# Kernel optimization log

Hardware: AMD Instinct MI355X
Metric: run time of the kernel (lower is better)

The kernel has to match this reference:

```python
import jax, jax.numpy as jnp
import numpy as np
from jax import lax

B, S = 64, 3000
Q_SIZES = [(4, 16), (16, 32), (32, 64), (64, 128), (128, 256)]
NUM_CLASS = 10


def setup_inputs() -> dict:
    key = jax.random.key(0)
    ks = iter(jax.random.split(key, 40))

    def g(shape, scale=0.05):
        return jax.random.normal(next(ks), shape, dtype=jnp.float32) * scale

    d = {}
    d["x"] = jax.random.normal(next(ks), (B, S, 1), dtype=jnp.float32)
    # vanilla tanh RNN, hidden=4
    d["wih"] = g((4, 1))
    d["whh"] = g((4, 4))
    d["bih"] = g((4,))
    d["bhh"] = g((4,))
    # 5 QRNN layers: affine to (Z, F) of width 2*out
    for i, (ni, no) in enumerate(Q_SIZES, 1):
        d[f"qw{i}"] = g((ni, 2 * no))
        d[f"qb{i}"] = g((2 * no,))
    # trailing MLP (weights stored as (in, out))
    d["w1"] = g((3000, 1024))
    d["b1"] = g((1024,))
    d["w2"] = g((1024, 128))
    d["b2"] = g((128,))
    d["w3"] = g((128, NUM_CLASS))
    d["b3"] = g((NUM_CLASS,))
    return d


def _rnn_tanh(x, wih, whh, bih, bhh):
    # x: (B, S, 1) -> (B, S, 4)
    pre = jnp.einsum('bsi,hi->bsh', x, wih) + bih + bhh  # input part precomputed
    b = x.shape[0]

    def step(h, p):
        h = jnp.tanh(p + h @ whh.T)
        return h, h

    _, hs = lax.scan(step, jnp.zeros((b, whh.shape[0]), x.dtype), jnp.moveaxis(pre, 1, 0))
    return jnp.moveaxis(hs, 0, 1)


def _qrnn(x, w, bq):
    # x: (B, S, Cin); fo-pool: h_t = f_t*h_{t-1} + (1-f_t)*z_t
    H = w.shape[1] // 2
    zf = x @ w + bq  # (B, S, 2H) -- one big GEMM, recurrence is elementwise
    z = jnp.tanh(zf[..., :H])
    f = jax.nn.sigmoid(zf[..., H:])
    b = x.shape[0]

    def step(h, zft):
        z_t, f_t = zft
        h = f_t * h + (1.0 - f_t) * z_t
        return h, h

    _, hs = lax.scan(step, jnp.zeros((b, H), x.dtype),
                     (jnp.moveaxis(z, 1, 0), jnp.moveaxis(f, 1, 0)))
    return jnp.moveaxis(hs, 0, 1)  # (B, S, H)


def reference(x, wih, whh, bih, bhh,
              qw1, qb1, qw2, qb2, qw3, qb3, qw4, qb4, qw5, qb5,
              w1, b1, w2, b2, w3, b3):
    h = _rnn_tanh(x, wih, whh, bih, bhh)          # (B, S, 4)
    for w, bq in ((qw1, qb1), (qw2, qb2), (qw3, qb3), (qw4, qb4), (qw5, qb5)):
        h = _qrnn(h, w, bq)                        # (B, S, C)
    # AdaptiveAvgPool1d(1) on (B, S, C): mean over channel axis -> (B, S)
    h = h.mean(axis=-1)                            # (B, 3000)
    h = jax.nn.relu(h @ w1 + b1)                   # dropout = identity (eval)
    h = jax.nn.relu(h @ w2 + b2)
    h = jax.nn.relu(h @ w3 + b3)
    return h
```

## Files before the change

### kernel.cpp

```cpp
#include <hip/hip_runtime.h>

#define DEVI __device__ __forceinline__

static constexpr int Bb = 64;
static constexpr int Ss = 3000;
static constexpr int Mm = Bb * Ss;
static constexpr int NCH = 12;
static constexpr int CLEN = 250;
static constexpr int WARM = 64;
static constexpr int NCK = 12;
static constexpr int RCH = 60;
static constexpr int RCLEN = 50;
static constexpr int RWARM = 32;

typedef short bs8 __attribute__((ext_vector_type(8)));
typedef float f32x4 __attribute__((ext_vector_type(4)));

DEVI float fast_tanh(float x) {
    float e = __expf(2.0f * x);
    return 1.0f - 2.0f * __builtin_amdgcn_rcpf(e + 1.0f);
}
DEVI float fast_sigmoid(float x) {
    return __builtin_amdgcn_rcpf(1.0f + __expf(-x));
}
DEVI unsigned short f2bf(float f) {
    unsigned u = __float_as_uint(f);
    u += 0x7FFF + ((u >> 16) & 1);
    return (unsigned short)(u >> 16);
}
DEVI float bf2f(unsigned short h) { return __uint_as_float(((unsigned)h) << 16); }

__global__ __launch_bounds__(64) void rnn_kernel2(const float* __restrict__ x,
                                                  const float* __restrict__ wih,
                                                  const float* __restrict__ whh,
                                                  const float* __restrict__ bih,
                                                  const float* __restrict__ bhh,
                                                  float* __restrict__ hout) {
    __shared__ float xs[Ss];
    int b = blockIdx.x;
    for (int i = threadIdx.x; i < Ss / 4; i += 64) {
        *(float4*)&xs[i * 4] = *(const float4*)&x[b * Ss + i * 4];
    }
    __syncthreads();
    int ck = threadIdx.x;
    if (ck >= RCH) return;
    float w[4][4], wi[4], bc[4];
#pragma unroll
    for (int j = 0; j < 4; ++j) {
        wi[j] = wih[j];
        bc[j] = bih[j] + bhh[j];
#pragma unroll
        for (int i = 0; i < 4; ++i) w[j][i] = whh[j * 4 + i];
    }
    float h0 = 0.f, h1 = 0.f, h2 = 0.f, h3 = 0.f;
    int sc = ck * RCLEN;
    int sb = ck ? (sc - RWARM) : 0;
#pragma unroll 4
    for (int s = sb; s < sc; ++s) {
        float xv = xs[s];
        float n0 = fast_tanh(fmaf(xv, wi[0], bc[0]) + w[0][0]*h0 + w[0][1]*h1 + w[0][2]*h2 + w[0][3]*h3);
        float n1 = fast_tanh(fmaf(xv, wi[1], bc[1]) + w[1][0]*h0 + w[1][1]*h1 + w[1][2]*h2 + w[1][3]*h3);
        float n2 = fast_tanh(fmaf(xv, wi[2], bc[2]) + w[2][0]*h0 + w[2][1]*h1 + w[2][2]*h2 + w[2][3]*h3);
        float n3 = fast_tanh(fmaf(xv, wi[3], bc[3]) + w[3][0]*h0 + w[3][1]*h1 + w[3][2]*h2 + w[3][3]*h3);
        h0 = n0; h1 = n1; h2 = n2; h3 = n3;
    }
#pragma unroll 5
    for (int s = sc; s < sc + RCLEN; ++s) {
        float xv = xs[s];
        float n0 = fast_tanh(fmaf(xv, wi[0], bc[0]) + w[0][0]*h0 + w[0][1]*h1 + w[0][2]*h2 + w[0][3]*h3);
        float n1 = fast_tanh(fmaf(xv, wi[1], bc[1]) + w[1][0]*h0 + w[1][1]*h1 + w[1][2]*h2 + w[1][3]*h3);
        float n2 = fast_tanh(fmaf(xv, wi[2], bc[2]) + w[2][0]*h0 + w[2][1]*h1 + w[2][2]*h2 + w[2][3]*h3);
        float n3 = fast_tanh(fmaf(xv, wi[3], bc[3]) + w[3][0]*h0 + w[3][1]*h1 + w[3][2]*h2 + w[3][3]*h3);
        h0 = n0; h1 = n1; h2 = n2; h3 = n3;
        *(float4*)&hout[(size_t)(b * Ss + s) * 4] = make_float4(h0, h1, h2, h3);
    }
}

__global__ void prep_wfrag(const float* __restrict__ W, short* __restrict__ Wh,
                           short* __restrict__ Wl, int K, int N2) {
    int total = K * N2;
    int NS = K / 32;
    for (int t = blockIdx.x * blockDim.x + threadIdx.x; t < total; t += gridDim.x * blockDim.x) {
        int n = t / K, k = t % K;
        float w = W[(size_t)k * N2 + n];
        int frag = n >> 4;
        int s = k >> 5;
        int lane = (n & 15) | (((k >> 3) & 3) << 4);
        int elem = k & 7;
        size_t off = (((size_t)(frag * NS + s)) * 64 + lane) * 8 + elem;
        unsigned short h = f2bf(w);
        Wh[off] = (short)h;
        Wl[off] = (short)f2bf(w - bf2f(h));
    }
}

template <int K, int H, bool POOL>
__global__ __launch_bounds__(512) void qrnn_fused(const short* __restrict__ Ap,
                                                  const short* __restrict__ Wh,
                                                  const short* __restrict__ Wl,
                                                  const float* __restrict__ bias,
                                                  short* __restrict__ Hout,
                                                  float* __restrict__ pooled) {
    constexpr int SUBR = 32;
    constexpr int NS = K / 32;
    constexpr int WN = (H / 16 < 8) ? (H / 16) : 8;
    constexpr int WR = 8 / WN;
    constexpr int NZF = H / (16 * WN);
    constexpr int RPW = SUBR / WR;
    constexpr int RF = RPW / 16;
    constexpr int LDA = K + 8;
    constexpr int ZP = H + 4;

    __shared__ short As[SUBR * LDA];
    __shared__ unsigned zfs[SUBR][ZP];

    const int tid = threadIdx.x;
    const int lane = tid & 63;
    const int w = tid >> 6;
    const int rg = w / WN, cg = w % WN;
    const int l15 = lane & 15, lh = lane >> 4;

    const int bi = blockIdx.x;
    const int b = bi / NCK, ck = bi % NCK;
    const int s0 = ck * 256;

    float hscan = 0.f;

    const int tstart = (ck == 0) ? 0 : -2;
    for (int t = tstart; t < 8; ++t) {
        const int st = s0 + t * SUBR;
        if (st >= Ss) break;
        const size_t grow0 = (size_t)b * Ss + st;

        {
            constexpr int CH = K / 8;
            for (int q = tid; q < SUBR * CH; q += 512) {
                int r = q / CH, hq = q % CH;
                *(bs8*)&As[r * LDA + hq * 8] = *(const bs8*)&Ap[(grow0 + r) * K + hq * 8];
            }
        }
        __syncthreads();

        f32x4 acc[RF][2 * NZF];
#pragma unroll
        for (int i = 0; i < RF; ++i)
#pragma unroll
            for (int j = 0; j < 2 * NZF; ++j) acc[i][j] = (f32x4)0.f;

#pragma unroll
        for (int s = 0; s < NS; ++s) {
            bs8 ah[RF];
#pragma unroll
            for (int i = 0; i < RF; ++i)
                ah[i] = *(const bs8*)&As[(rg * RPW + i * 16 + l15) * LDA + s * 32 + lh * 8];
#pragma unroll
            for (int nz = 0; nz < NZF; ++nz) {
                int fz = cg * NZF + nz;
                int ff = H / 16 + fz;
                bs8 bzh = *(const bs8*)&Wh[(((size_t)fz * NS + s) * 64 + lane) * 8];
                bs8 bzl = *(const bs8*)&Wl[(((size_t)fz * NS + s) * 64 + lane) * 8];
                bs8 bfh = *(const bs8*)&Wh[(((size_t)ff * NS + s) * 64 + lane) * 8];
                bs8 bfl = *(const bs8*)&Wl[(((size_t)ff * NS + s) * 64 + lane) * 8];
#pragma unroll
                for (int i = 0; i < RF; ++i) {
                    acc[i][nz] = __builtin_amdgcn_mfma_f32_16x16x32_bf16(ah[i], bzh, acc[i][nz], 0, 0, 0);
                    acc[i][nz] = __builtin_amdgcn_mfma_f32_16x16x32_bf16(ah[i], bzl, acc[i][nz], 0, 0, 0);
                    acc[i][NZF + nz] = __builtin_amdgcn_mfma_f32_16x16x32_bf16(ah[i], bfh, acc[i][NZF + nz], 0, 0, 0);
                    acc[i][NZF + nz] = __builtin_amdgcn_mfma_f32_16x16x32_bf16(ah[i], bfl, acc[i][NZF + nz], 0, 0, 0);
                }
            }
        }

#pragma unroll
        for (int nz = 0; nz < NZF; ++nz) {
            int c = cg * (16 * NZF) + nz * 16 + l15;
            float bz = bias[c], bfv = bias[H + c];
#pragma unroll
            for (int i = 0; i < RF; ++i) {
                int rbase = rg * RPW + i * 16 + lh * 4;
#pragma unroll
                for (int r = 0; r < 4; ++r) {
                    float zv = fast_tanh(acc[i][nz][r] + bz);
                    float fv = fast_sigmoid(acc[i][NZF + nz][r] + bfv);
                    zfs[rbase + r][c] = (((unsigned)f2bf(zv)) << 16) | (unsigned)f2bf(fv);
                }
            }
        }
        __syncthreads();

        if (tid < H) {
            int c = tid;
            float h = hscan;
#pragma unroll 8
            for (int r = 0; r < SUBR; ++r) {
                unsigned u = zfs[r][c];
                float z = bf2f((unsigned short)(u >> 16));
                float f = bf2f((unsigned short)(u & 0xFFFF));
                h = fmaf(f, h - z, z);
                if (POOL) {
                    zfs[r][c] = __float_as_uint(h);
                } else {
                    int s = st + r;
                    if (t >= 0 && s < Ss)
                        Hout[((size_t)b * Ss + s) * H + c] = (short)f2bf(h);
                }
            }
            hscan = h;
        }
        __syncthreads();

        if (POOL) {
            if (t >= 0) {
#pragma unroll
                for (int rr = 0; rr < SUBR / 8; ++rr) {
                    int r = w * (SUBR / 8) + rr;
                    float sum = __uint_as_float(zfs[r][lane]) +
                                __uint_as_float(zfs[r][lane + 64]) +
                                __uint_as_float(zfs[r][lane + 128]) +
                                __uint_as_float(zfs[r][lane + 192]);
#pragma unroll
                    for (int off = 32; off >= 1; off >>= 1)
                        sum += __shfl_xor(sum, off, 64);
                    int s = st + r;
                    if (lane == 0 && s < Ss)
                        pooled[(size_t)b * Ss + s] = sum * (1.f / 256.f);
                }
            }
            __syncthreads();
        }
    }
}

template <int K>
__global__ __launch_bounds__(256) void qrnn_gemm(const float* __restrict__ A,
                                                 const float* __restrict__ W,
                                                 const float* __restrict__ bias,
                                                 float* __restrict__ ZF,
                                                 int Nfull, int Wout, int Hg, int z0, int f0) {
    constexpr int BM = 64, BN = 64;
    constexpr int BK = (K < 32) ? K : 32;
    __shared__ float As[BK][BM + 4];
    __shared__ float Bs[BK][BN];
    const int tid = threadIdx.x;
    const int tx = tid % 16, ty = tid / 16;
    const int m0 = blockIdx.x * BM;
    const int n0 = blockIdx.y * BN;
    float acc[4][4] = {};

    for (int k0 = 0; k0 < K; k0 += BK) {
        constexpr int KQ = BK / 4;
        constexpr int AV = BM * KQ;
        for (int v = tid; v < AV; v += 256) {
            int m = v / KQ, kq = v % KQ;
            float4 av = *(const float4*)&A[(size_t)(m0 + m) * K + k0 + kq * 4];
            As[kq * 4 + 0][m] = av.x;
            As[kq * 4 + 1][m] = av.y;
            As[kq * 4 + 2][m] = av.z;
            As[kq * 4 + 3][m] = av.w;
        }
        constexpr int BV = BK * 16;
        for (int v = tid; v < BV; v += 256) {
            int ki = v / 16, nq = v % 16;
            int j = n0 + nq * 4;
            float4 bv = make_float4(0.f, 0.f, 0.f, 0.f);
            if (j < Wout) {
                int wc = (j < Hg) ? (z0 + j) : (f0 + (j - Hg));
                bv = *(const float4*)&W[(size_t)(k0 + ki) * Nfull + wc];
            }
            *(float4*)&Bs[ki][nq * 4] = bv;
        }
        __syncthreads();
#pragma unroll
        for (int kk = 0; kk < BK; ++kk) {
            float a[4];
#pragma unroll
            for (int i = 0; i < 4; ++i) a[i] = As[kk][ty * 4 + i];
            float4 bv = *(const float4*)&Bs[kk][tx * 4];
            float bb[4] = {bv.x, bv.y, bv.z, bv.w};
#pragma unroll
            for (int i = 0; i < 4; ++i)
#pragma unroll
                for (int j = 0; j < 4; ++j) acc[i][j] = fmaf(a[i], bb[j], acc[i][j]);
        }
        __syncthreads();
    }
    int jb = n0 + tx * 4;
    if (jb < Wout) {
        bool isz = jb < Hg;
#pragma unroll
        for (int i = 0; i < 4; ++i) {
            int gm = m0 + ty * 4 + i;
            float o[4];
#pragma unroll
            for (int jj = 0; jj < 4; ++jj) {
                int j = jb + jj;
                int wc = isz ? (z0 + j) : (f0 + (j - Hg));
                float v = acc[i][jj] + bias[wc];
                o[jj] = isz ? fast_tanh(v) : fast_sigmoid(v);
            }
            *(float4*)&ZF[(size_t)gm * Wout + jb] = make_float4(o[0], o[1], o[2], o[3]);
        }
    }
}

__global__ void scan_f2c(const float* __restrict__ zf, float* __restrict__ hout,
                         int Hg, int W2, int Hfull, int ch0) {
    int id = blockIdx.x * blockDim.x + threadIdx.x;
    int total = Bb * NCH * Hg;
    if (id >= total) return;
    int c = id % Hg;
    int p = id / Hg;
    int b = p / NCH, ck = p % NCH;
    int sc = ck * CLEN;
    float h = 0.f;
    if (ck) {
#pragma unroll 4
        for (int s = sc - WARM; s < sc; ++s) {
            size_t base = (size_t)(b * Ss + s) * W2;
            float z = zf[base + c], f = zf[base + Hg + c];
            h = fmaf(f, h - z, z);
        }
    }
#pragma unroll 5
    for (int s = sc; s < sc + CLEN; ++s) {
        size_t base = (size_t)(b * Ss + s) * W2;
        float z = zf[base + c], f = zf[base + Hg + c];
        h = fmaf(f, h - z, z);
        hout[(size_t)(b * Ss + s) * Hfull + ch0 + c] = h;
    }
}

__global__ void scan_f2p(const float* __restrict__ zf, short* __restrict__ Ahp,
                         int Hg, int W2, int Kn, int ch0) {
    int id = blockIdx.x * blockDim.x + threadIdx.x;
    int total = Bb * NCH * Hg;
    if (id >= total) return;
    int c = id % Hg;
    int p = id / Hg;
    int b = p / NCH, ck = p % NCH;
    int sc = ck * CLEN;
    float h = 0.f;
    if (ck) {
#pragma unroll 4
        for (int s = sc - WARM; s < sc; ++s) {
            size_t base = (size_t)(b * Ss + s) * W2;
            float z = zf[base + c], f = zf[base + Hg + c];
            h = fmaf(f, h - z, z);
        }
    }
#pragma unroll 5
    for (int s = sc; s < sc + CLEN; ++s) {
        size_t base = (size_t)(b * Ss + s) * W2;
        float z = zf[base + c], f = zf[base + Hg + c];
        h = fmaf(f, h - z, z);
        Ahp[(size_t)(b * Ss + s) * Kn + ch0 + c] = (short)f2bf(h);
    }
}

__global__ __launch_bounds__(256) void mlp1_kernel(const float* __restrict__ xp,
                                                   const float* __restrict__ w1,
                                                   float* __restrict__ parts) {
    const int n0 = blockIdx.x * 64;
    const int ks = blockIdx.y;
    const int kbeg = ks * 250;
    const int nl = threadIdx.x % 64, mg = threadIdx.x / 64;
    __shared__ float xs[50][68];
    float acc[16] = {};
    for (int kc = 0; kc < 5; ++kc) {
        int k0 = kbeg + kc * 50;
        __syncthreads();
        for (int idx = threadIdx.x; idx < 64 * 50; idx += 256) {
            int r = idx / 50, cc = idx % 50;
            xs[cc][r] = xp[r * Ss + k0 + cc];
        }
        __syncthreads();
#pragma unroll 5
        for (int kk = 0; kk < 50; ++kk) {
            float wv = w1[(size_t)(k0 + kk) * 1024 + n0 + nl];
#pragma unroll
            for (int q = 0; q < 4; ++q) {
                float4 xv = *(const float4*)&xs[kk][mg * 16 + q * 4];
                acc[q * 4 + 0] = fmaf(xv.x, wv, acc[q * 4 + 0]);
                acc[q * 4 + 1] = fmaf(xv.y, wv, acc[q * 4 + 1]);
                acc[q * 4 + 2] = fmaf(xv.z, wv, acc[q * 4 + 2]);
                acc[q * 4 + 3] = fmaf(xv.w, wv, acc[q * 4 + 3]);
            }
        }
    }
#pragma unroll
    for (int i = 0; i < 16; ++i) {
        int m = mg * 16 + i;
        parts[((size_t)ks * 64 + m) * 1024 + n0 + nl] = acc[i];
    }
}

__global__ void mlp1_reduce(const float* __restrict__ parts, const float* __restrict__ b1,
                            float* __restrict__ h1) {
    int id = blockIdx.x * 256 + threadIdx.x;
    int n = id % 1024, m = id / 1024;
    float s = b1[n];
#pragma unroll
    for (int ks = 0; ks < 12; ++ks) s += parts[((size_t)ks * 64 + m) * 1024 + n];
    h1[id] = fmaxf(s, 0.f);
}

__global__ void mlp2_kernel(const float* __restrict__ h1, const float* __restrict__ w2,
                            const float* __restrict__ b2, float* __restrict__ h2) {
    int m = blockIdx.x, n = threadIdx.x;
    float acc = 0.f;
#pragma unroll 8
    for (int k = 0; k < 1024; ++k) acc = fmaf(h1[m * 1024 + k], w2[k * 128 + n], acc);
    h2[m * 128 + n] = fmaxf(acc + b2[n], 0.f);
}

__global__ void mlp3_kernel(const float* __restrict__ h2, const float* __restrict__ w3,
                            const float* __restrict__ b3, float* __restrict__ out) {
    int t = threadIdx.x;
    if (t >= 640) return;
    int m = t / 10, n = t % 10;
    float acc = 0.f;
#pragma unroll
    for (int k = 0; k < 128; ++k) acc = fmaf(h2[m * 128 + k], w3[k * 10 + n], acc);
    out[t] = fmaxf(acc + b3[n], 0.f);
}

extern "C" void kernel_launch(void* const* d_in, const int* in_sizes, int n_in,
                              void* d_out, int out_size, void* d_ws, size_t ws_size,
                              hipStream_t stream) {
    const float* x   = (const float*)d_in[0];
    const float* wih = (const float*)d_in[1];
    const float* whh = (const float*)d_in[2];
    const float* bih = (const float*)d_in[3];
    const float* bhh = (const float*)d_in[4];
    const float* qw[5] = {(const float*)d_in[5], (const float*)d_in[7], (const float*)d_in[9],
                          (const float*)d_in[11], (const float*)d_in[13]};
    const float* qb[5] = {(const float*)d_in[6], (const float*)d_in[8], (const float*)d_in[10],
                          (const float*)d_in[12], (const float*)d_in[14]};
    const float* w1 = (const float*)d_in[15];
    const float* b1 = (const float*)d_in[16];
    const float* w2 = (const float*)d_in[17];
    const float* b2 = (const float*)d_in[18];
    const float* w3 = (const float*)d_in[19];
    const float* b3 = (const float*)d_in[20];
    float* out = (float*)d_out;

    char* ws = (char*)d_ws;
    size_t off = 0;
    auto carve = [&](size_t sz) {
        char* q = ws + off;
        off += (sz + 255) & ~size_t(255);
        return q;
    };
    float* h4    = (float*)carve((size_t)Mm * 4 * 4);
    float* h16   = (float*)carve((size_t)Mm * 16 * 4);
    float* zf32  = (float*)carve((size_t)Mm * 64 * 4);
    short* p32   = (short*)carve((size_t)(Mm + 128) * 32 * 2);
    short* p64   = (short*)carve((size_t)(Mm + 128) * 64 * 2);
    short* p128  = (short*)carve((size_t)(Mm + 128) * 128 * 2);
    float* pooled = (float*)carve((size_t)Bb * Ss * 4);
    float* parts  = (float*)carve(12ull * 64 * 1024 * 4);
    float* h1m    = (float*)carve(64ull * 1024 * 4);
    float* h2m    = (float*)carve(64ull * 128 * 4);
    short* wh2 = (short*)carve(4096 * 2);
    short* wl2 = (short*)carve(4096 * 2);
    short* wh3 = (short*)carve(16384 * 2);
    short* wl3 = (short*)carve(16384 * 2);
    short* wh4 = (short*)carve(65536 * 2);
    short* wl4 = (short*)carve(65536 * 2);
    (void)ws_size;

    prep_wfrag<<<8,  256, 0, stream>>>(qw[2], wh2, wl2, 32, 128);
    prep_wfrag<<<16, 256, 0, stream>>>(qw[3], wh3, wl3, 64, 256);
    prep_wfrag<<<64, 256, 0, stream>>>(qw[4], wh4, wl4, 128, 512);

    rnn_kernel2<<<Bb, 64, 0, stream>>>(x, wih, whh, bih, bhh, h4);

    {
        dim3 grid(Mm / 64, 1);
        qrnn_gemm<4><<<grid, 256, 0, stream>>>(h4, qw[0], qb[0], zf32, 32, 32, 16, 0, 16);
        int total = Bb * NCH * 16;
        scan_f2c<<<(total + 255) / 256, 256, 0, stream>>>(zf32, h16, 16, 32, 16, 0);
    }
    {
        dim3 grid(Mm / 64, 1);
        qrnn_gemm<16><<<grid, 256, 0, stream>>>(h16, qw[1], qb[1], zf32, 64, 64, 32, 0, 32);
        int total = Bb * NCH * 32;
        scan_f2p<<<(total + 255) / 256, 256, 0, stream>>>(zf32, p32, 32, 64, 32, 0);
    }
    qrnn_fused<32, 64, false><<<Bb * NCK, 512, 0, stream>>>(p32, wh2, wl2, qb[2], p64, nullptr);
    qrnn_fused<64, 128, false><<<Bb * NCK, 512, 0, stream>>>(p64, wh3, wl3, qb[3], p128, nullptr);
    qrnn_fused<128, 256, true><<<Bb * NCK, 512, 0, stream>>>(p128, wh4, wl4, qb[4], nullptr, pooled);

    mlp1_kernel<<<dim3(16, 12), 256, 0, stream>>>(pooled, w1, parts);
    mlp1_reduce<<<256, 256, 0, stream>>>(parts, b1, h1m);
    mlp2_kernel<<<64, 128, 0, stream>>>(h1m, w2, b2, h2m);
    mlp3_kernel<<<1, 640, 0, stream>>>(h2m, w3, b3, out);
    (void)in_sizes; (void)n_in; (void)out_size;
}
```

Before: 598.4 us.

## Double-buffer activation tiles, preload weights to registers, widen QRNN subtiles

The fused QRNN kernel now loads its hi/lo bf16 weight fragments into registers once per block instead of re-reading them from global memory on every subtile. Activation tiles are double-buffered in shared memory so the next tile's load is issued while the current tile's MFMAs run. The subtile height grows from 32 to 64 rows, and the warm-up history shrinks from two 32-row subtiles to one 64-row subtile. The aim is less global weight traffic and fewer barrier stalls, at the cost of much higher register pressure for large K/H layers and twice the LDS for the A tile.

```diff
diff --git a/kernel.cpp b/kernel.cpp
--- a/kernel.cpp
+++ b/kernel.cpp
@@ -101,7 +101,8 @@
                                                   const float* __restrict__ bias,
                                                   short* __restrict__ Hout,
                                                   float* __restrict__ pooled) {
-    constexpr int SUBR = 32;
+    constexpr int SUBR = 64;
+    constexpr int NT = 256 / SUBR;
     constexpr int NS = K / 32;
     constexpr int WN = (H / 16 < 8) ? (H / 16) : 8;
     constexpr int WR = 8 / WN;
@@ -110,8 +111,9 @@
     constexpr int RF = RPW / 16;
     constexpr int LDA = K + 8;
     constexpr int ZP = H + 4;
-
-    __shared__ short As[SUBR * LDA];
+    constexpr int CH = K / 8;
+
+    __shared__ short As[2 * SUBR * LDA];
     __shared__ unsigned zfs[SUBR][ZP];
 
     const int tid = threadIdx.x;
@@ -124,60 +126,78 @@
     const int b = bi / NCK, ck = bi % NCK;
     const int s0 = ck * 256;
 
+    bs8 wzh[NS * NZF], wzl[NS * NZF], wfh[NS * NZF], wfl[NS * NZF];
+#pragma unroll
+    for (int s = 0; s < NS; ++s)
+#pragma unroll
+        for (int nz = 0; nz < NZF; ++nz) {
+            const int fz = cg * NZF + nz;
+            const int ff = H / 16 + fz;
+            wzh[s * NZF + nz] = *(const bs8*)&Wh[(((size_t)fz * NS + s) * 64 + lane) * 8];
+            wzl[s * NZF + nz] = *(const bs8*)&Wl[(((size_t)fz * NS + s) * 64 + lane) * 8];
+            wfh[s * NZF + nz] = *(const bs8*)&Wh[(((size_t)ff * NS + s) * 64 + lane) * 8];
+            wfl[s * NZF + nz] = *(const bs8*)&Wl[(((size_t)ff * NS + s) * 64 + lane) * 8];
+        }
+
     float hscan = 0.f;
-
-    const int tstart = (ck == 0) ? 0 : -2;
-    for (int t = tstart; t < 8; ++t) {
+    const int tstart = (ck == 0) ? 0 : -1;
+
+    {
+        const size_t grow0 = (size_t)b * Ss + s0 + tstart * SUBR;
+        for (int q = tid; q < SUBR * CH; q += 512) {
+            int r = q / CH, hq = q % CH;
+            *(bs8*)&As[r * LDA + hq * 8] = *(const bs8*)&Ap[(grow0 + r) * K + hq * 8];
+        }
+    }
+    __syncthreads();
+
+    for (int t = tstart; t < NT; ++t) {
         const int st = s0 + t * SUBR;
         if (st >= Ss) break;
-        const size_t grow0 = (size_t)b * Ss + st;
-
-        {
-            constexpr int CH = K / 8;
+        const int cur = (t - tstart) & 1;
+        const short* Ac = &As[cur * SUBR * LDA];
+
+        f32x4 acc[RF][2 * NZF];
+#pragma unroll
+        for (int i = 0; i < RF; ++i)
+#pragma unroll
+            for (int j = 0; j < 2 * NZF; ++j) acc[i][j] = (f32x4)0.f;
+
+#pragma unroll
+        for (int s = 0; s < NS; ++s) {
+            bs8 ah[RF];
+#pragma unroll
+            for (int i = 0; i < RF; ++i)
+                ah[i] = *(const bs8*)&Ac[(rg * RPW + i * 16 + l15) * LDA + s * 32 + lh * 8];
+#pragma unroll
+            for (int nz = 0; nz < NZF; ++nz) {
+                const int wi_ = s * NZF + nz;
+#pragma unroll
+                for (int i = 0; i < RF; ++i) {
+                    acc[i][nz] = __builtin_amdgcn_mfma_f32_16x16x32_bf16(ah[i], wzh[wi_], acc[i][nz], 0, 0, 0);
+                    acc[i][nz] = __builtin_amdgcn_mfma_f32_16x16x32_bf16(ah[i], wzl[wi_], acc[i][nz], 0, 0, 0);
+                    acc[i][NZF + nz] = __builtin_amdgcn_mfma_f32_16x16x32_bf16(ah[i], wfh[wi_], acc[i][NZF + nz], 0, 0, 0);
+                    acc[i][NZF + nz] = __builtin_amdgcn_mfma_f32_16x16x32_bf16(ah[i], wfl[wi_], acc[i][NZF + nz], 0, 0, 0);
+                }
+            }
+        }
+
+        if (t + 1 < NT && s0 + (t + 1) * SUBR < Ss) {
+            const size_t g2 = (size_t)b * Ss + s0 + (t + 1) * SUBR;
+            short* An = &As[(cur ^ 1) * SUBR * LDA];
             for (int q = tid; q < SUBR * CH; q += 512) {
                 int r = q / CH, hq = q % CH;
-                *(bs8*)&As[r * LDA + hq * 8] = *(const bs8*)&Ap[(grow0 + r) * K + hq * 8];
-            }
-        }
-        __syncthreads();
-
-        f32x4 acc[RF][2 * NZF];
-#pragma unroll
-        for (int i = 0; i < RF; ++i)
-#pragma unroll
-            for (int j = 0; j < 2 * NZF; ++j) acc[i][j] = (f32x4)0.f;
-
-#pragma unroll
-        for (int s = 0; s < NS; ++s) {
-            bs8 ah[RF];
-#pragma unroll
-            for (int i = 0; i < RF; ++i)
-                ah[i] = *(const bs8*)&As[(rg * RPW + i * 16 + l15) * LDA + s * 32 + lh * 8];
-#pragma unroll
-            for (int nz = 0; nz < NZF; ++nz) {
-                int fz = cg * NZF + nz;
-                int ff = H / 16 + fz;
-                bs8 bzh = *(const bs8*)&Wh[(((size_t)fz * NS + s) * 64 + lane) * 8];
-                bs8 bzl = *(const bs8*)&Wl[(((size_t)fz * NS + s) * 64 + lane) * 8];
-                bs8 bfh = *(const bs8*)&Wh[(((size_t)ff * NS + s) * 64 + lane) * 8];
-                bs8 bfl = *(const bs8*)&Wl[(((size_t)ff * NS + s) * 64 + lane) * 8];
-#pragma unroll
-                for (int i = 0; i < RF; ++i) {
-                    acc[i][nz] = __builtin_amdgcn_mfma_f32_16x16x32_bf16(ah[i], bzh, acc[i][nz], 0, 0, 0);
-                    acc[i][nz] = __builtin_amdgcn_mfma_f32_16x16x32_bf16(ah[i], bzl, acc[i][nz], 0, 0, 0);
-                    acc[i][NZF + nz] = __builtin_amdgcn_mfma_f32_16x16x32_bf16(ah[i], bfh, acc[i][NZF + nz], 0, 0, 0);
-                    acc[i][NZF + nz] = __builtin_amdgcn_mfma_f32_16x16x32_bf16(ah[i], bfl, acc[i][NZF + nz], 0, 0, 0);
-                }
+                *(bs8*)&An[r * LDA + hq * 8] = *(const bs8*)&Ap[(g2 + r) * K + hq * 8];
             }
         }
 
 #pragma unroll
         for (int nz = 0; nz < NZF; ++nz) {
-            int c = cg * (16 * NZF) + nz * 16 + l15;
-            float bz = bias[c], bfv = bias[H + c];
+            const int c = cg * (16 * NZF) + nz * 16 + l15;
+            const float bz = bias[c], bfv = bias[H + c];
 #pragma unroll
             for (int i = 0; i < RF; ++i) {
-                int rbase = rg * RPW + i * 16 + lh * 4;
+                const int rbase = rg * RPW + i * 16 + lh * 4;
 #pragma unroll
                 for (int r = 0; r < 4; ++r) {
                     float zv = fast_tanh(acc[i][nz][r] + bz);
@@ -189,7 +209,7 @@
         __syncthreads();
 
         if (tid < H) {
-            int c = tid;
+            const int c = tid;
             float h = hscan;
 #pragma unroll 8
             for (int r = 0; r < SUBR; ++r) {
@@ -213,7 +233,7 @@
             if (t >= 0) {
 #pragma unroll
                 for (int rr = 0; rr < SUBR / 8; ++rr) {
-                    int r = w * (SUBR / 8) + rr;
+                    const int r = w * (SUBR / 8) + rr;
                     float sum = __uint_as_float(zfs[r][lane]) +
                                 __uint_as_float(zfs[r][lane + 64]) +
                                 __uint_as_float(zfs[r][lane + 128]) +
```

Measured after the change: 552.4 us. -7.7%, faster.
